# Kernel optimization log

Hardware: AMD Instinct MI355X
Metric: run time of the kernel (lower is better)

The kernel has to match this reference:

```python
import jax, jax.numpy as jnp
import numpy as np

# Module configuration (from init_kwargs)
NLAT_IN, NLON_IN = 181, 360
NLAT_OUT, NLON_OUT = 361, 720
KSIZE = 3            # kernel_size of piecewise-linear basis with kernel_shape=3
CIN, COUT = 16, 16   # groups=1 -> groupsize = CIN
NNZ = 8192           # nonzeros in the precomputed psi tensor
B = 1


def setup_inputs() -> dict:
    key = jax.random.key(0)
    ks = jax.random.split(key, 6)
    x = jax.random.normal(ks[0], (B, CIN, NLAT_IN, NLON_IN), dtype=jnp.float32)
    # weight init: sqrt(1/groupsize) * basis init factors * randn
    scale = np.float32(np.sqrt(1.0 / CIN))
    weight = scale * jax.random.normal(ks[1], (COUT, CIN, KSIZE), dtype=jnp.float32)
    bias = jnp.zeros((COUT,), dtype=jnp.float32)
    # synthetic COO psi tensor (geometry-free but structurally identical)
    ker_idx = jax.random.randint(ks[2], (NNZ,), 0, KSIZE, dtype=jnp.int32)
    row_idx = jax.random.randint(ks[3], (NNZ,), 0, NLAT_IN, dtype=jnp.int32)
    col_idx = jax.random.randint(ks[4], (NNZ,), 0, NLAT_OUT * NLON_OUT, dtype=jnp.int32)
    vals = jax.random.uniform(ks[5], (NNZ,), dtype=jnp.float32) * (100.0 / NNZ)
    return {"x": x, "weight": weight, "bias": bias,
            "ker_idx": ker_idx, "row_idx": row_idx, "col_idx": col_idx, "vals": vals}


def reference(x, weight, bias, ker_idx, row_idx, col_idx, vals):
    """DISCO transpose conv on S2: channel-mix einsum, then sparse
    gather-multiply-scatter (adjoint of the longitude-shift-equivariant
    sparse contraction). col_idx encodes (out_lat, lon_offset)."""
    Bb, Cin, H, W = x.shape            # (B, C_in, nlat_in, nlon_in)
    Cout, gs, K = weight.shape
    pscale = NLON_OUT // W             # exact p-shift upsampling factor

    # 1) channel mixing with per-kernel-basis weights (groups=1)
    xw = jnp.einsum('bcxy,ock->bokxy', x, weight)   # [B, Cout, K, nlat_in, nlon_in]

    # 2) gather rows referenced by the sparse psi tensor and scale by vals
    g = xw[:, :, ker_idx, row_idx, :] * vals[None, None, :, None]  # [B, Cout, NNZ, W]

    # 3) scatter-add: each nonzero (k, tin, (tout, p)) contributes the whole
    #    longitude ring of input lat tin to output lat tout at lons (p + po*pscale)
    hi = col_idx // NLON_OUT                      # output latitude  [NNZ]
    p = col_idx % NLON_OUT                        # longitude offset [NNZ]
    lon = (p[:, None] + jnp.arange(W, dtype=p.dtype)[None, :] * pscale) % NLON_OUT  # [NNZ, W]
    flat = (hi[:, None] * NLON_OUT + lon).reshape(-1)  # [NNZ*W]

    out = jnp.zeros((Bb, Cout, NLAT_OUT * NLON_OUT), dtype=x.dtype)
    out = out.at[:, :, flat].add(g.reshape(Bb, Cout, -1))
    out = out.reshape(Bb, Cout, NLAT_OUT, NLON_OUT)
    return out + bias[None, :, None, None]
```

## Files before the change

### kernel.cpp

```cpp
#include <hip/hip_runtime.h>

#define H_IN   181
#define W_IN   360
#define NLAT   361
#define NLON   720
#define CIN    16
#define COUT   16
#define KSZ    3
#define NNZ    8192
#define MAXB   64
#define XPLANE (H_IN * W_IN)

__global__ __launch_bounds__(384) void fused_disco_kernel(
    const float* __restrict__ x,
    const float* __restrict__ w,
    const float* __restrict__ bias,
    const int*   __restrict__ ker_idx,
    const int*   __restrict__ row_idx,
    const int*   __restrict__ col_idx,
    const float* __restrict__ vals,
    float* __restrict__ out)
{
    const int ho  = blockIdx.x >> 1;
    const int pe  = blockIdx.x & 1;
    const int tid = threadIdx.x;

    __shared__ int   s_cnt;
    __shared__ int   s_xrow[MAXB];
    __shared__ int   s_pk[MAXB];
    __shared__ float s_v[MAXB];

    if (tid == 0) s_cnt = 0;
    __syncthreads();

    for (int n = tid; n < NNZ; n += 384) {
        const int c  = col_idx[n];
        const int hi = c / NLON;
        const int p  = c - hi * NLON;
        if (hi == ho && (p & 1) == pe) {
            const int slot = atomicAdd(&s_cnt, 1);
            if (slot < MAXB) {
                s_xrow[slot] = row_idx[n] * W_IN;
                s_pk[slot]   = p | (ker_idx[n] << 12);
                s_v[slot]    = vals[n];
            }
        }
    }
    __syncthreads();
    const int cnt = (s_cnt < MAXB) ? s_cnt : MAXB;

    if (tid >= 360) return;
    const int lon = 2 * tid + pe;

    float g0[CIN], g1[CIN], g2[CIN];
#pragma unroll
    for (int c = 0; c < CIN; ++c) { g0[c] = 0.f; g1[c] = 0.f; g2[c] = 0.f; }

    for (int e = 0; e < cnt; ++e) {
        const int   pk = __builtin_amdgcn_readfirstlane(s_pk[e]);
        const int   xr = __builtin_amdgcn_readfirstlane(s_xrow[e]);
        const float v  = __uint_as_float(
                           __builtin_amdgcn_readfirstlane(__float_as_uint(s_v[e])));
        const int p = pk & 0xfff;
        const int k = pk >> 12;

        int d = lon - p;
        if (d < 0) d += NLON;
        const int y = d >> 1;

        const float* xp = x + xr + y;
        float xv[CIN];
#pragma unroll
        for (int c = 0; c < CIN; ++c) xv[c] = xp[c * XPLANE];

        if (k == 0) {
#pragma unroll
            for (int c = 0; c < CIN; ++c) g0[c] += v * xv[c];
        } else if (k == 1) {
#pragma unroll
            for (int c = 0; c < CIN; ++c) g1[c] += v * xv[c];
        } else {
#pragma unroll
            for (int c = 0; c < CIN; ++c) g2[c] += v * xv[c];
        }
    }

#pragma unroll
    for (int co = 0; co < COUT; ++co) {
        float s = bias[co];
#pragma unroll
        for (int c = 0; c < CIN; ++c) {
            const int wb = (co * CIN + c) * KSZ;
            s += g0[c] * w[wb + 0];
            s += g1[c] * w[wb + 1];
            s += g2[c] * w[wb + 2];
        }
        out[((size_t)co * NLAT + ho) * NLON + lon] = s;
    }
}

extern "C" void kernel_launch(void* const* d_in, const int* in_sizes, int n_in,
                              void* d_out, int out_size, void* d_ws, size_t ws_size,
                              hipStream_t stream) {
    const float* x       = (const float*)d_in[0];
    const float* weight  = (const float*)d_in[1];
    const float* bias    = (const float*)d_in[2];
    const int*   ker_idx = (const int*)d_in[3];
    const int*   row_idx = (const int*)d_in[4];
    const int*   col_idx = (const int*)d_in[5];
    const float* vals    = (const float*)d_in[6];
    float* out = (float*)d_out;

    (void)d_ws; (void)ws_size;

    fused_disco_kernel<<<NLAT * 2, 384, 0, stream>>>(
        x, weight, bias, ker_idx, row_idx, col_idx, vals, out);
}
```

Measured before the change: 115.7 us.

## Split rows into halves, bucket nonzeros per kernel basis, unroll gather pairs

```diff
diff --git a/kernel.cpp b/kernel.cpp
--- a/kernel.cpp
+++ b/kernel.cpp
@@ -8,10 +8,20 @@
 #define COUT   16
 #define KSZ    3
 #define NNZ    8192
-#define MAXB   64
 #define XPLANE (H_IN * W_IN)
+#define MAXK   32
+#define NPAIR  (NLAT * 2)
+#define GRID   1456
 
-__global__ __launch_bounds__(384) void fused_disco_kernel(
+
+static __device__ __forceinline__ int rfl_i(int i) {
+    return __builtin_amdgcn_readfirstlane(i);
+}
+static __device__ __forceinline__ float rfl_f(float f) {
+    return __uint_as_float(__builtin_amdgcn_readfirstlane(__float_as_uint(f)));
+}
+
+__global__ __launch_bounds__(192) void fused_disco_kernel(
     const float* __restrict__ x,
     const float* __restrict__ w,
     const float* __restrict__ bias,
@@ -21,69 +31,91 @@
     const float* __restrict__ vals,
     float* __restrict__ out)
 {
-    const int ho  = blockIdx.x >> 1;
-    const int pe  = blockIdx.x & 1;
-    const int tid = threadIdx.x;
+    const int bid   = blockIdx.x;
+    const int r     = bid & 7;
+    const int inner = bid >> 3;
+    const int pe    = inner & 1;
+    const int p     = (inner >> 1) * 8 + r;
+    if (p >= NPAIR) return;
+    const int ho   = p >> 1;
+    const int half = p & 1;
+    const int tid  = threadIdx.x;
 
-    __shared__ int   s_cnt;
-    __shared__ int   s_xrow[MAXB];
-    __shared__ int   s_pk[MAXB];
-    __shared__ float s_v[MAXB];
+    __shared__ int   s_ck[3];
+    __shared__ int   s_ps[3 * MAXK];
+    __shared__ int   s_xr[3 * MAXK];
+    __shared__ float s_v [3 * MAXK];
 
-    if (tid == 0) s_cnt = 0;
+    if (tid < 3) s_ck[tid] = 0;
     __syncthreads();
 
-    for (int n = tid; n < NNZ; n += 384) {
+    for (int n = tid; n < NNZ; n += 192) {
         const int c  = col_idx[n];
         const int hi = c / NLON;
-        const int p  = c - hi * NLON;
-        if (hi == ho && (p & 1) == pe) {
-            const int slot = atomicAdd(&s_cnt, 1);
-            if (slot < MAXB) {
-                s_xrow[slot] = row_idx[n] * W_IN;
-                s_pk[slot]   = p | (ker_idx[n] << 12);
-                s_v[slot]    = vals[n];
-            }
+        if (hi != ho) continue;
+        const int pf = c - hi * NLON;
+        if ((pf & 1) != pe) continue;
+        const int k    = ker_idx[n];
+        const int slot = atomicAdd(&s_ck[k], 1);
+        if (slot < MAXK) {
+            s_ps[k * MAXK + slot] = pf >> 1;
+            s_xr[k * MAXK + slot] = row_idx[n] * W_IN;
+            s_v [k * MAXK + slot] = vals[n];
         }
     }
     __syncthreads();
-    const int cnt = (s_cnt < MAXB) ? s_cnt : MAXB;
 
-    if (tid >= 360) return;
-    const int lon = 2 * tid + pe;
+    if (tid < 3) {
+        int c = s_ck[tid] < MAXK ? s_ck[tid] : MAXK;
+        if (c & 1) {
+            s_ps[tid * MAXK + c] = 0;
+            s_xr[tid * MAXK + c] = 0;
+            s_v [tid * MAXK + c] = 0.f;
+            ++c;
+        }
+        s_ck[tid] = c;
+    }
+    __syncthreads();
+
+    const int ck0 = rfl_i(s_ck[0]);
+    const int ck1 = rfl_i(s_ck[1]);
+    const int ck2 = rfl_i(s_ck[2]);
+
+    if (tid >= 180) return;
+    const int lonIdx = half * 180 + tid;
+    const int lon    = 2 * lonIdx + pe;
 
     float g0[CIN], g1[CIN], g2[CIN];
 #pragma unroll
     for (int c = 0; c < CIN; ++c) { g0[c] = 0.f; g1[c] = 0.f; g2[c] = 0.f; }
 
-    for (int e = 0; e < cnt; ++e) {
-        const int   pk = __builtin_amdgcn_readfirstlane(s_pk[e]);
-        const int   xr = __builtin_amdgcn_readfirstlane(s_xrow[e]);
-        const float v  = __uint_as_float(
-                           __builtin_amdgcn_readfirstlane(__float_as_uint(s_v[e])));
-        const int p = pk & 0xfff;
-        const int k = pk >> 12;
+#define SEG(K, CK, GK)                                                          \
+    for (int e = 0; e < (CK); e += 2) {                                         \
+        const int   ps0 = rfl_i(s_ps[(K) * MAXK + e]);                          \
+        const int   xr0 = rfl_i(s_xr[(K) * MAXK + e]);                          \
+        const float v0  = rfl_f(s_v [(K) * MAXK + e]);                          \
+        const int   ps1 = rfl_i(s_ps[(K) * MAXK + e + 1]);                      \
+        const int   xr1 = rfl_i(s_xr[(K) * MAXK + e + 1]);                      \
+        const float v1  = rfl_f(s_v [(K) * MAXK + e + 1]);                      \
+        int y0 = lonIdx - ps0; y0 += (y0 >> 31) & 360;                          \
+        int y1 = lonIdx - ps1; y1 += (y1 >> 31) & 360;                          \
+        const unsigned i0 = (unsigned)(xr0 + y0);                               \
+        const unsigned i1 = (unsigned)(xr1 + y1);                               \
+        float a0[CIN], a1[CIN];                                                 \
+        _Pragma("unroll")                                                       \
+        for (int c = 0; c < CIN; ++c) a0[c] = x[i0 + (unsigned)(c * XPLANE)];   \
+        _Pragma("unroll")                                                       \
+        for (int c = 0; c < CIN; ++c) a1[c] = x[i1 + (unsigned)(c * XPLANE)];   \
+        _Pragma("unroll")                                                       \
+        for (int c = 0; c < CIN; ++c) GK[c] += v0 * a0[c];                      \
+        _Pragma("unroll")                                                       \
+        for (int c = 0; c < CIN; ++c) GK[c] += v1 * a1[c];                      \
+    }
 
-        int d = lon - p;
-        if (d < 0) d += NLON;
-        const int y = d >> 1;
-
-        const float* xp = x + xr + y;
-        float xv[CIN];
-#pragma unroll
-        for (int c = 0; c < CIN; ++c) xv[c] = xp[c * XPLANE];
-
-        if (k == 0) {
-#pragma unroll
-            for (int c = 0; c < CIN; ++c) g0[c] += v * xv[c];
-        } else if (k == 1) {
-#pragma unroll
-            for (int c = 0; c < CIN; ++c) g1[c] += v * xv[c];
-        } else {
-#pragma unroll
-            for (int c = 0; c < CIN; ++c) g2[c] += v * xv[c];
-        }
-    }
+    SEG(0, ck0, g0)
+    SEG(1, ck1, g1)
+    SEG(2, ck2, g2)
+#undef SEG
 
 #pragma unroll
     for (int co = 0; co < COUT; ++co) {
@@ -113,6 +145,6 @@
 
     (void)d_ws; (void)ws_size;
 
-    fused_disco_kernel<<<NLAT * 2, 384, 0, stream>>>(
+    fused_disco_kernel<<<GRID, 192, 0, stream>>>(
         x, weight, bias, ker_idx, row_idx, col_idx, vals, out);
 }
```

After: 119.0 us. +2.9%, slower.
